# Kernel tuning notes

Hardware: AMD Instinct MI355X
Metric: run time of the kernel (lower is better)

The kernel has to match this reference:

```python
import jax, jax.numpy as jnp
import numpy as np


def setup_inputs() -> dict:
    key = jax.random.key(0)
    x = jax.random.normal(key, (64, 512, 40, 40), dtype=jnp.float32)
    return {"x": x}


def reference(x) -> jnp.ndarray:
    # unfold(k=3, pad=1, stride=1) followed by fold back to (40, 40) is an
    # overlap-sum: each output pixel is the sum of its 3x3 neighborhood
    # (zero-padded at borders) == depthwise conv with a 3x3 ones kernel.
    C = x.shape[1]
    kernel = jnp.ones((C, 1, 3, 3), dtype=x.dtype)  # depthwise ones kernel
    return jax.lax.conv_general_dilated(
        x, kernel,
        window_strides=(1, 1),
        padding=((1, 1), (1, 1)),
        dimension_numbers=("NCHW", "OIHW", "NCHW"),
        feature_group_count=C,
    )
```

## Files before the change

kernel.cpp:

```cpp
#include <hip/hip_runtime.h>


#define PLANE_ELEMS 1600
#define PLANE_VEC4  400
#define W 40

__global__ __launch_bounds__(256) void overlap_sum_3x3(
    const float* __restrict__ in, float* __restrict__ out)
{
    __shared__ float s_a[PLANE_ELEMS];
    __shared__ float s_h[PLANE_ELEMS];

    const int t = threadIdx.x;
    const size_t plane_off = (size_t)blockIdx.x * PLANE_ELEMS;

    const float4* src4 = reinterpret_cast<const float4*>(in + plane_off);
    float4* s_a4 = reinterpret_cast<float4*>(s_a);
    s_a4[t] = src4[t];
    if (t < PLANE_VEC4 - 256) s_a4[t + 256] = src4[t + 256];
    __syncthreads();

    #pragma unroll
    for (int i = t; i < PLANE_ELEMS; i += 256) {
        const int x = i % W;
        const float v = s_a[i];
        const float l = (x > 0)     ? s_a[i - 1] : 0.0f;
        const float r = (x < W - 1) ? s_a[i + 1] : 0.0f;
        s_h[i] = l + v + r;
    }
    __syncthreads();

    #pragma unroll
    for (int i = t; i < PLANE_ELEMS; i += 256) {
        const float v = s_h[i];
        const float u = (i >= W)                 ? s_h[i - W] : 0.0f;
        const float d = (i < PLANE_ELEMS - W)    ? s_h[i + W] : 0.0f;
        s_a[i] = u + v + d;
    }
    __syncthreads();

    float4* dst4 = reinterpret_cast<float4*>(out + plane_off);
    dst4[t] = s_a4[t];
    if (t < PLANE_VEC4 - 256) dst4[t + 256] = s_a4[t + 256];
}

extern "C" void kernel_launch(void* const* d_in, const int* in_sizes, int n_in,
                              void* d_out, int out_size, void* d_ws, size_t ws_size,
                              hipStream_t stream) {
    const float* x = (const float*)d_in[0];
    float* out = (float*)d_out;
    const int n_planes = in_sizes[0] / PLANE_ELEMS;
    overlap_sum_3x3<<<n_planes, 256, 0, stream>>>(x, out);
}
```

Measured before the change: 76.48 us.

## Stream plane rows through registers with lane shuffles instead of LDS staging

Each group of 10 lanes now owns one 40x40 plane and walks it row by row, with 24 planes per 256-thread block. The horizontal 3-tap sum uses wave shuffles across float4 neighbours, and the vertical sum keeps a rolling three-row window in registers. This removes the shared-memory round trips and the block-wide barriers. In exchange, 4 of 64 lanes per wave sit idle, there are fewer blocks, and each load instruction covers scattered 160-byte row segments from six planes.

```diff
diff --git a/kernel.cpp b/kernel.cpp
--- a/kernel.cpp
+++ b/kernel.cpp
@@ -1,47 +1,79 @@
 #include <hip/hip_runtime.h>
 
 
+#define W 40
+#define H 40
+#define VEC_PER_ROW 10
 #define PLANE_ELEMS 1600
-#define PLANE_VEC4  400
-#define W 40
+#define GROUPS_PER_WAVE 6
+#define WAVES_PER_BLOCK 4
+#define PLANES_PER_BLOCK (GROUPS_PER_WAVE * WAVES_PER_BLOCK)
 
 __global__ __launch_bounds__(256) void overlap_sum_3x3(
-    const float* __restrict__ in, float* __restrict__ out)
+    const float* __restrict__ in, float* __restrict__ out, int n_planes)
 {
-    __shared__ float s_a[PLANE_ELEMS];
-    __shared__ float s_h[PLANE_ELEMS];
+    const int t    = threadIdx.x;
+    const int wave = t >> 6;
+    const int lane = t & 63;
+    const int group = lane / 10;
+    const int x4    = lane - group * 10;
+    if (group >= GROUPS_PER_WAVE) return;
 
-    const int t = threadIdx.x;
-    const size_t plane_off = (size_t)blockIdx.x * PLANE_ELEMS;
+    const int plane = blockIdx.x * PLANES_PER_BLOCK + wave * GROUPS_PER_WAVE + group;
+    if (plane >= n_planes) return;
 
-    const float4* src4 = reinterpret_cast<const float4*>(in + plane_off);
-    float4* s_a4 = reinterpret_cast<float4*>(s_a);
-    s_a4[t] = src4[t];
-    if (t < PLANE_VEC4 - 256) s_a4[t + 256] = src4[t + 256];
-    __syncthreads();
+    const float4* __restrict__ src =
+        reinterpret_cast<const float4*>(in + (size_t)plane * PLANE_ELEMS) + x4;
+    float4* __restrict__ dst =
+        reinterpret_cast<float4*>(out + (size_t)plane * PLANE_ELEMS) + x4;
 
-    #pragma unroll
-    for (int i = t; i < PLANE_ELEMS; i += 256) {
-        const int x = i % W;
-        const float v = s_a[i];
-        const float l = (x > 0)     ? s_a[i - 1] : 0.0f;
-        const float r = (x < W - 1) ? s_a[i + 1] : 0.0f;
-        s_h[i] = l + v + r;
+    const bool has_left  = (x4 != 0);
+    const bool has_right = (x4 != VEC_PER_ROW - 1);
+
+    float4 hm1 = make_float4(0.f, 0.f, 0.f, 0.f);
+    float4 h0;
+    {
+        const float4 v = src[0];
+        float lf = __shfl_up(v.w, 1);
+        float rt = __shfl_down(v.x, 1);
+        if (!has_left)  lf = 0.f;
+        if (!has_right) rt = 0.f;
+        h0.x = lf  + v.x + v.y;
+        h0.y = v.x + v.y + v.z;
+        h0.z = v.y + v.z + v.w;
+        h0.w = v.z + v.w + rt;
     }
-    __syncthreads();
 
-    #pragma unroll
-    for (int i = t; i < PLANE_ELEMS; i += 256) {
-        const float v = s_h[i];
-        const float u = (i >= W)                 ? s_h[i - W] : 0.0f;
-        const float d = (i < PLANE_ELEMS - W)    ? s_h[i + W] : 0.0f;
-        s_a[i] = u + v + d;
+    #pragma unroll 4
+    for (int y = 1; y < H; ++y) {
+        const float4 v = src[y * VEC_PER_ROW];
+        float lf = __shfl_up(v.w, 1);
+        float rt = __shfl_down(v.x, 1);
+        if (!has_left)  lf = 0.f;
+        if (!has_right) rt = 0.f;
+        float4 h1;
+        h1.x = lf  + v.x + v.y;
+        h1.y = v.x + v.y + v.z;
+        h1.z = v.y + v.z + v.w;
+        h1.w = v.z + v.w + rt;
+
+        float4 o;
+        o.x = hm1.x + h0.x + h1.x;
+        o.y = hm1.y + h0.y + h1.y;
+        o.z = hm1.z + h0.z + h1.z;
+        o.w = hm1.w + h0.w + h1.w;
+        dst[(y - 1) * VEC_PER_ROW] = o;
+
+        hm1 = h0;
+        h0  = h1;
     }
-    __syncthreads();
 
-    float4* dst4 = reinterpret_cast<float4*>(out + plane_off);
-    dst4[t] = s_a4[t];
-    if (t < PLANE_VEC4 - 256) dst4[t + 256] = s_a4[t + 256];
+    float4 o;
+    o.x = hm1.x + h0.x;
+    o.y = hm1.y + h0.y;
+    o.z = hm1.z + h0.z;
+    o.w = hm1.w + h0.w;
+    dst[(H - 1) * VEC_PER_ROW] = o;
 }
 
 extern "C" void kernel_launch(void* const* d_in, const int* in_sizes, int n_in,
@@ -50,5 +82,6 @@
     const float* x = (const float*)d_in[0];
     float* out = (float*)d_out;
     const int n_planes = in_sizes[0] / PLANE_ELEMS;
-    overlap_sum_3x3<<<n_planes, 256, 0, stream>>>(x, out);
+    const int grid = (n_planes + PLANES_PER_BLOCK - 1) / PLANES_PER_BLOCK;
+    overlap_sum_3x3<<<grid, 256, 0, stream>>>(x, out, n_planes);
 }
```

Result: slower. 99.82 us (+30.5%).

## Vectorize 3x3 overlap-sum with float4 register passes and direct global store

Applied to the files above, without the earlier changes.

Each thread now handles float4 chunks. It keeps the loaded values in registers, builds the horizontal sum from its own float4 plus one neighbor element on each side, and does the vertical sum on float4 shared-memory rows. The final pass writes straight to global memory, which removes the third barrier and the shared-memory round trip before the store. This cuts scalar LDS traffic and the modulo work. The kernel is already dominated by memory bandwidth (roughly 420 MB moved), so the gain may be small.

```diff
diff --git a/kernel.cpp b/kernel.cpp
--- a/kernel.cpp
+++ b/kernel.cpp
@@ -1,47 +1,74 @@
 #include <hip/hip_runtime.h>
 
 
-#define PLANE_ELEMS 1600
-#define PLANE_VEC4  400
-#define W 40
+#define NV 400
+#define ROW4 10
+
+__device__ __forceinline__ float4 hsum4(const float4 c, float lf, float rt) {
+    float4 h;
+    h.x = lf  + c.x + c.y;
+    h.y = c.x + c.y + c.z;
+    h.z = c.y + c.z + c.w;
+    h.w = c.z + c.w + rt;
+    return h;
+}
 
 __global__ __launch_bounds__(256) void overlap_sum_3x3(
     const float* __restrict__ in, float* __restrict__ out)
 {
-    __shared__ float s_a[PLANE_ELEMS];
-    __shared__ float s_h[PLANE_ELEMS];
+    __shared__ float4 s_a[NV];
+    __shared__ float4 s_h[NV];
 
     const int t = threadIdx.x;
-    const size_t plane_off = (size_t)blockIdx.x * PLANE_ELEMS;
+    const size_t po = (size_t)blockIdx.x * NV;
+    const float4* __restrict__ src = reinterpret_cast<const float4*>(in) + po;
+    float4*       __restrict__ dst = reinterpret_cast<float4*>(out) + po;
 
-    const float4* src4 = reinterpret_cast<const float4*>(in + plane_off);
-    float4* s_a4 = reinterpret_cast<float4*>(s_a);
-    s_a4[t] = src4[t];
-    if (t < PLANE_VEC4 - 256) s_a4[t + 256] = src4[t + 256];
+    const bool two = (t < NV - 256);
+    float4 v0 = src[t];
+    float4 v1;
+    s_a[t] = v0;
+    if (two) { v1 = src[t + 256]; s_a[t + 256] = v1; }
     __syncthreads();
 
-    #pragma unroll
-    for (int i = t; i < PLANE_ELEMS; i += 256) {
-        const int x = i % W;
-        const float v = s_a[i];
-        const float l = (x > 0)     ? s_a[i - 1] : 0.0f;
-        const float r = (x < W - 1) ? s_a[i + 1] : 0.0f;
-        s_h[i] = l + v + r;
+    const int x40 = t % ROW4;
+    float lf0 = (x40 > 0)        ? s_a[t - 1].w : 0.0f;
+    float rt0 = (x40 < ROW4 - 1) ? s_a[t + 1].x : 0.0f;
+    float4 h0 = hsum4(v0, lf0, rt0);
+    s_h[t] = h0;
+
+    float4 h1;
+    if (two) {
+        const int j  = t + 256;
+        const int x41 = j % ROW4;
+        float lf1 = (x41 > 0)        ? s_a[j - 1].w : 0.0f;
+        float rt1 = (x41 < ROW4 - 1) ? s_a[j + 1].x : 0.0f;
+        h1 = hsum4(v1, lf1, rt1);
+        s_h[j] = h1;
     }
     __syncthreads();
 
-    #pragma unroll
-    for (int i = t; i < PLANE_ELEMS; i += 256) {
-        const float v = s_h[i];
-        const float u = (i >= W)                 ? s_h[i - W] : 0.0f;
-        const float d = (i < PLANE_ELEMS - W)    ? s_h[i + W] : 0.0f;
-        s_a[i] = u + v + d;
+    {
+        float4 o = h0;
+        if (t >= ROW4) {
+            const float4 u = s_h[t - ROW4];
+            o.x += u.x; o.y += u.y; o.z += u.z; o.w += u.w;
+        }
+        const float4 d = s_h[t + ROW4];
+        o.x += d.x; o.y += d.y; o.z += d.z; o.w += d.w;
+        dst[t] = o;
     }
-    __syncthreads();
-
-    float4* dst4 = reinterpret_cast<float4*>(out + plane_off);
-    dst4[t] = s_a4[t];
-    if (t < PLANE_VEC4 - 256) dst4[t + 256] = s_a4[t + 256];
+    if (two) {
+        const int j = t + 256;
+        float4 o = h1;
+        const float4 u = s_h[j - ROW4];
+        o.x += u.x; o.y += u.y; o.z += u.z; o.w += u.w;
+        if (j < NV - ROW4) {
+            const float4 d = s_h[j + ROW4];
+            o.x += d.x; o.y += d.y; o.z += d.z; o.w += d.w;
+        }
+        dst[j] = o;
+    }
 }
 
 extern "C" void kernel_launch(void* const* d_in, const int* in_sizes, int n_in,
@@ -49,6 +76,6 @@
                               hipStream_t stream) {
     const float* x = (const float*)d_in[0];
     float* out = (float*)d_out;
-    const int n_planes = in_sizes[0] / PLANE_ELEMS;
+    const int n_planes = in_sizes[0] / (NV * 4);
     overlap_sum_3x3<<<n_planes, 256, 0, stream>>>(x, out);
 }
```

Measured after the change: 76.87 us. No clear change (+0.5%).
